# Performance work log

Measured on AMD Instinct MI355X. Metric: run time of the kernel, lower is better.

## Reference

```python
import jax, jax.numpy as jnp
import numpy as np
from jax import lax

# dims
B_SZ, H_SZ, W_SZ = 2, 48, 48
D_MODEL = 192
SSM_RATIO = 2.0
D_PROJ = int(SSM_RATIO * D_MODEL)        # 384
C_INNER = 2 * D_PROJ                     # 768 = K * D_IN
K_GRP = 4
D_IN = C_INNER // K_GRP                  # 192 (= d_inner, channel_divide=2)
N_STATE = 16
R_RANK = 12                              # ceil(192/16)


def setup_inputs() -> dict:
    key = jax.random.key(0)
    ks = jax.random.split(key, 12)
    x = jax.random.normal(ks[0], (B_SZ, H_SZ, W_SZ, 2 * D_MODEL), jnp.float32)
    in_proj_w = jax.random.normal(ks[1], (C_INNER, 2 * D_MODEL), jnp.float32) * 0.02
    conv_w = jax.random.normal(ks[2], (C_INNER, 1, 3, 3), jnp.float32) * 0.1
    conv_b = jnp.zeros((C_INNER,), jnp.float32)
    x_proj_weight = jax.random.normal(ks[3], (K_GRP, R_RANK + 2 * N_STATE, D_IN), jnp.float32) * 0.05
    dt_projs_weight = jax.random.normal(ks[4], (K_GRP, D_IN, R_RANK), jnp.float32) * (R_RANK ** -0.5)
    # faithful dt bias init: softplus^{-1}(dt) with dt ~ logU[1e-3, 1e-1]
    dt = jnp.exp(jax.random.uniform(ks[5], (K_GRP, D_IN)) * (np.log(0.1) - np.log(0.001)) + np.log(0.001))
    dt = jnp.clip(dt, 1e-4, None)
    dt_projs_bias = dt + jnp.log(-jnp.expm1(-dt))
    # A_log init: log(arange(1..N)) per channel, K copies merged
    A_logs = jnp.log(jnp.tile(jnp.arange(1, N_STATE + 1, dtype=jnp.float32)[None, :], (K_GRP * D_IN, 1)))
    Ds = jnp.ones((K_GRP * D_IN,), jnp.float32)
    out_norm_w = jnp.ones((C_INNER,), jnp.float32)
    out_norm_b = jnp.zeros((C_INNER,), jnp.float32)
    out_proj_w = jax.random.normal(ks[6], (2 * D_MODEL, C_INNER), jnp.float32) * 0.02
    return dict(x=x, in_proj_w=in_proj_w, conv_w=conv_w, conv_b=conv_b,
                x_proj_weight=x_proj_weight, dt_projs_weight=dt_projs_weight,
                dt_projs_bias=dt_projs_bias, A_logs=A_logs, Ds=Ds,
                out_norm_w=out_norm_w, out_norm_b=out_norm_b, out_proj_w=out_proj_w)


def _ss2d(x, in_proj_w, conv_w, conv_b, x_proj_weight, dt_projs_weight,
          dt_projs_bias, A_logs, Ds, out_norm_w, out_norm_b, out_proj_w):
    B, H, W, _ = x.shape
    C = in_proj_w.shape[0]
    K = x_proj_weight.shape[0]
    d = C // K
    N = A_logs.shape[1]
    R = dt_projs_weight.shape[2]
    L = H * W

    # in_proj (disable_z: no gating split)
    xz = jnp.einsum('bhwc,oc->bhwo', x, in_proj_w)
    xc = xz.transpose(0, 3, 1, 2)  # [B,C,H,W]
    # depthwise 3x3 conv + SiLU
    xc = lax.conv_general_dilated(xc, conv_w, (1, 1), 'SAME', feature_group_count=C)
    xc = xc + conv_b[None, :, None, None]
    xc = xc * jax.nn.sigmoid(xc)

    # CrossScanS: split channels into K groups, each scanned in its own direction
    ch = xc.reshape(B, K, d, H, W)
    f0 = ch[:, 0].reshape(B, d, L)                                        # row-major fwd
    f1 = ch[:, 1].transpose(0, 1, 3, 2).reshape(B, d, L)                  # col-major fwd
    f2 = jnp.flip(ch[:, 2].reshape(B, d, L), -1)                          # row-major rev
    f3 = jnp.flip(ch[:, 3].transpose(0, 1, 3, 2).reshape(B, d, L), -1)    # col-major rev
    xs = jnp.stack([f0, f1, f2, f3], axis=1)  # [B,K,d,L]

    # input-dependent dt/B/C projections
    x_dbl = jnp.einsum('bkdl,kcd->bkcl', xs, x_proj_weight)
    dts, Bs, Cs = jnp.split(x_dbl, [R, R + N], axis=2)  # [B,K,R,L],[B,K,N,L],[B,K,N,L]
    dts = jnp.einsum('bkrl,kdr->bkdl', dts, dt_projs_weight) + dt_projs_bias[None, :, :, None]

    # force_fp32 selective scan with delta_softplus
    u = xs.astype(jnp.float32)
    dts = jax.nn.softplus(dts.astype(jnp.float32))
    Bs = Bs.astype(jnp.float32)
    Cs = Cs.astype(jnp.float32)
    A = -jnp.exp(A_logs.astype(jnp.float32)).reshape(K, d, N)  # [K,d,N]

    def step(h, inp):
        u_t, dt_t, B_t, C_t = inp  # [B,K,d],[B,K,d],[B,K,N],[B,K,N]
        h = h * jnp.exp(dt_t[..., None] * A) + (dt_t * u_t)[..., None] * B_t[:, :, None, :]
        y_t = jnp.einsum('bkdn,bkn->bkd', h, C_t)
        return h, y_t

    inps = (u.transpose(3, 0, 1, 2), dts.transpose(3, 0, 1, 2),
            Bs.transpose(3, 0, 1, 2), Cs.transpose(3, 0, 1, 2))
    h0 = jnp.zeros((B, K, d, N), jnp.float32)
    _, ys = lax.scan(step, h0, inps)          # ys: [L,B,K,d]
    ys = ys.transpose(1, 2, 3, 0)             # [B,K,d,L]
    ys = ys + Ds.astype(jnp.float32).reshape(K, d)[None, :, :, None] * u

    # CrossMergeS: undo each direction, concat channels back
    y0 = ys[:, 0]
    y1 = ys[:, 1].reshape(B, d, W, H).transpose(0, 1, 3, 2).reshape(B, d, L)
    y2 = jnp.flip(ys[:, 2], -1)
    y3 = jnp.flip(ys[:, 3], -1).reshape(B, d, W, H).transpose(0, 1, 3, 2).reshape(B, d, L)
    y = jnp.concatenate([y0, y1, y2, y3], axis=1).reshape(B, C, H, W).transpose(0, 2, 3, 1)

    # out_norm: LayerNorm over channels
    mu = jnp.mean(y, -1, keepdims=True)
    var = jnp.mean(jnp.square(y - mu), -1, keepdims=True)
    y = (y - mu) * lax.rsqrt(var + 1e-5) * out_norm_w + out_norm_b

    out = jnp.einsum('bhwc,oc->bhwo', y.astype(x.dtype), out_proj_w)
    return out


def reference(x, in_proj_w, conv_w, conv_b, x_proj_weight, dt_projs_weight,
              dt_projs_bias, A_logs, Ds, out_norm_w, out_norm_b, out_proj_w):
    return _ss2d(x, in_proj_w, conv_w, conv_b, x_proj_weight, dt_projs_weight,
                 dt_projs_bias, A_logs, Ds, out_norm_w, out_norm_b, out_proj_w)
```

## Files before the change

kernel.cpp:

```cpp
#include <hip/hip_runtime.h>
#include <hip/hip_bf16.h>

#define B_SZ   2
#define H_SZ   48
#define W_SZ   48
#define L_SZ   2304
#define CIN    768
#define KG     4
#define DI     192
#define NS     16
#define RR     12
#define XD     44
#define MTOK   4608
#define CL     16
#define NC     144

typedef __attribute__((ext_vector_type(8))) short short8;
typedef __attribute__((ext_vector_type(4))) float f32x4;

__device__ inline ushort f2b(float f) {
    uint u = __builtin_bit_cast(uint, f);
    u = (u + 0x7FFF + ((u >> 16) & 1)) >> 16;
    return (ushort)u;
}
__device__ inline float b2f(ushort b) {
    uint u = ((uint)b) << 16;
    return __builtin_bit_cast(float, u);
}
__device__ inline short8 f2b8(float4 a, float4 b) {
    short8 r;
    r[0] = (short)f2b(a.x); r[1] = (short)f2b(a.y);
    r[2] = (short)f2b(a.z); r[3] = (short)f2b(a.w);
    r[4] = (short)f2b(b.x); r[5] = (short)f2b(b.y);
    r[6] = (short)f2b(b.z); r[7] = (short)f2b(b.w);
    return r;
}

__device__ inline void gridbar(uint* bar, uint nb) {
    __syncthreads();
    if (threadIdx.x == 0) {
        uint g = __hip_atomic_load(&bar[1], __ATOMIC_RELAXED, __HIP_MEMORY_SCOPE_AGENT);
        uint a = __hip_atomic_fetch_add(&bar[0], 1u, __ATOMIC_ACQ_REL, __HIP_MEMORY_SCOPE_AGENT);
        if (a == nb - 1u) {
            __hip_atomic_store(&bar[0], 0u, __ATOMIC_RELAXED, __HIP_MEMORY_SCOPE_AGENT);
            __hip_atomic_store(&bar[1], g + 1u, __ATOMIC_RELEASE, __HIP_MEMORY_SCOPE_AGENT);
        } else {
            while (__hip_atomic_load(&bar[1], __ATOMIC_ACQUIRE, __HIP_MEMORY_SCOPE_AGENT) == g) {
                __builtin_amdgcn_s_sleep(8);
            }
        }
    }
    __syncthreads();
}

template<int TM, int TN, bool ABF, bool CBF>
__global__ __launch_bounds__(256) void gemm_tn(
        const void* __restrict__ Av, const float* __restrict__ Bw,
        void* __restrict__ Cv, int M, int N, int K) {
    __shared__ ushort As[TM][72];
    __shared__ ushort Bs[TN][72];
    constexpr int MF   = TM / 64;
    constexpr int NF   = TN / 16;
    constexpr int ANUM = TM / 32;
    constexpr int BNUM = TN / 32;
    const int tid  = threadIdx.x;
    const int lane = tid & 63;
    const int wave = tid >> 6;
    const int wrow = wave * (MF * 16);
    const int bm = blockIdx.y * TM, bn = blockIdx.x * TN;
    const int frow = lane & 15;
    const int fk   = (lane >> 4) * 8;
    const int orow = (lane >> 4) * 4;

    f32x4 acc[MF][NF] = {};

    for (int k0 = 0; k0 < K; k0 += 64) {
        short8 aval[ANUM];
#pragma unroll
        for (int i = 0; i < ANUM; ++i) {
            int idx = tid + i * 256;
            int row = idx >> 3, q = idx & 7;
            if (ABF) {
                aval[i] = *(const short8*)&((const ushort*)Av)[(size_t)(bm + row) * K + k0 + q * 8];
            } else {
                const float* ap = &((const float*)Av)[(size_t)(bm + row) * K + k0 + q * 8];
                aval[i] = f2b8(*(const float4*)ap, *(const float4*)(ap + 4));
            }
        }
        short8 bval[BNUM];
#pragma unroll
        for (int i = 0; i < BNUM; ++i) {
            int idx = tid + i * 256;
            int row = idx >> 3, q = idx & 7;
            const float* bp = &Bw[(size_t)(bn + row) * K + k0 + q * 8];
            bval[i] = f2b8(*(const float4*)bp, *(const float4*)(bp + 4));
        }

        __syncthreads();
#pragma unroll
        for (int i = 0; i < ANUM; ++i) {
            int idx = tid + i * 256;
            *(short8*)&As[idx >> 3][(idx & 7) * 8] = aval[i];
        }
#pragma unroll
        for (int i = 0; i < BNUM; ++i) {
            int idx = tid + i * 256;
            *(short8*)&Bs[idx >> 3][(idx & 7) * 8] = bval[i];
        }
        __syncthreads();

#pragma unroll
        for (int hf = 0; hf < 2; ++hf) {
            short8 af[MF], bf[NF];
#pragma unroll
            for (int mi = 0; mi < MF; ++mi)
                af[mi] = *(const short8*)&As[wrow + mi * 16 + frow][hf * 32 + fk];
#pragma unroll
            for (int ni = 0; ni < NF; ++ni)
                bf[ni] = *(const short8*)&Bs[ni * 16 + frow][hf * 32 + fk];
#pragma unroll
            for (int mi = 0; mi < MF; ++mi)
#pragma unroll
                for (int ni = 0; ni < NF; ++ni)
                    acc[mi][ni] = __builtin_amdgcn_mfma_f32_16x16x32_bf16(
                                      af[mi], bf[ni], acc[mi][ni], 0, 0, 0);
        }
    }

#pragma unroll
    for (int mi = 0; mi < MF; ++mi) {
        int rbase = bm + wrow + mi * 16 + orow;
#pragma unroll
        for (int ni = 0; ni < NF; ++ni) {
            int col = bn + ni * 16 + frow;
#pragma unroll
            for (int r = 0; r < 4; ++r) {
                if (CBF)
                    ((ushort*)Cv)[(size_t)(rbase + r) * N + col] = f2b(acc[mi][ni][r]);
                else
                    ((float*)Cv)[(size_t)(rbase + r) * N + col] = acc[mi][ni][r];
            }
        }
    }
}

__global__ __launch_bounds__(256) void conv_silu_scatter(
        const ushort* __restrict__ xzb, const float* __restrict__ cw,
        const float* __restrict__ cb, ushort* __restrict__ xsb) {
    int g = blockIdx.x * 256 + threadIdx.x;
    int c8 = g % 96;
    int pos = g / 96;
    int w = pos % W_SZ;
    int h = (pos / W_SZ) % H_SZ;
    int b = pos / (W_SZ * H_SZ);
    int c0 = c8 * 8;

    float wt[72];
    const float* cwp = &cw[c0 * 9];
#pragma unroll
    for (int i = 0; i < 18; ++i) {
        float4 v = *(const float4*)(cwp + i * 4);
        wt[i * 4 + 0] = v.x; wt[i * 4 + 1] = v.y;
        wt[i * 4 + 2] = v.z; wt[i * 4 + 3] = v.w;
    }
    float acc[8];
#pragma unroll
    for (int j = 0; j < 8; ++j) acc[j] = cb[c0 + j];

#pragma unroll
    for (int dh = -1; dh <= 1; ++dh) {
        int hh = h + dh;
        if (hh < 0 || hh >= H_SZ) continue;
#pragma unroll
        for (int dw = -1; dw <= 1; ++dw) {
            int ww = w + dw;
            if (ww < 0 || ww >= W_SZ) continue;
            int tap = (dh + 1) * 3 + (dw + 1);
            short8 xv = *(const short8*)&xzb[(size_t)((b * H_SZ + hh) * W_SZ + ww) * CIN + c0];
#pragma unroll
            for (int j = 0; j < 8; ++j)
                acc[j] = fmaf(b2f((ushort)xv[j]), wt[j * 9 + tap], acc[j]);
        }
    }

    float s[8];
#pragma unroll
    for (int j = 0; j < 8; ++j)
        s[j] = acc[j] * __builtin_amdgcn_rcpf(1.f + __expf(-acc[j]));

    int k = c0 / DI, d = c0 % DI;
    int lrow = h * W_SZ + w;
    int lcol = w * H_SZ + h;
    int l;
    if      (k == 0) l = lrow;
    else if (k == 1) l = lcol;
    else if (k == 2) l = L_SZ - 1 - lrow;
    else             l = L_SZ - 1 - lcol;
    float4 lo = {s[0], s[1], s[2], s[3]}, hi = {s[4], s[5], s[6], s[7]};
    *(short8*)&xsb[(size_t)((b * KG + k) * L_SZ + l) * DI + d] = f2b8(lo, hi);
}

__global__ __launch_bounds__(384) void xproj_dt_mfma(
        const ushort* __restrict__ xsb, const float* __restrict__ xpw,
        const float* __restrict__ dtw, const float* __restrict__ dtb,
        float* __restrict__ xdbl, ushort* __restrict__ dts_b) {
    __shared__ ushort Ws[48][200];
    __shared__ ushort Wd[192][40];
    __shared__ ushort dsh[32][40];

    const int tid  = threadIdx.x;
    const int lane = tid & 63;
    const int wave = tid >> 6;
    const int bm = blockIdx.x * 32;
    const int bk = blockIdx.y;
    const int k  = bk & 3;
    const int frow = lane & 15;
    const int fk   = (lane >> 4) * 8;
    const int orow = (lane >> 4) * 4;
    const int rg = wave & 1;
    const int cg = wave >> 1;

#pragma unroll
    for (int i = 0; i < 6; ++i) {
        int idx = tid + i * 384;
        int row = idx / 48, g = idx % 48;
        ushort4 u = {0, 0, 0, 0};
        if (row < XD) {
            float4 v = *(const float4*)&xpw[((size_t)(k * XD) + row) * 192 + g * 4];
            u.x = f2b(v.x); u.y = f2b(v.y); u.z = f2b(v.z); u.w = f2b(v.w);
        }
        *(ushort4*)&Ws[row][g * 4] = u;
    }
#pragma unroll
    for (int i = 0; i < 3; ++i) {
        int idx = tid + i * 384;
        if (idx < 960) {
            float4 z = {0.f, 0.f, 0.f, 0.f};
            *(float4*)&Wd[idx / 5][(idx % 5) * 8] = z;
        } else if (idx < 1120) {
            int j = idx - 960;
            float4 z = {0.f, 0.f, 0.f, 0.f};
            *(float4*)&dsh[j / 5][(j % 5) * 8] = z;
        }
    }
    __syncthreads();

#pragma unroll
    for (int i = 0; i < 6; ++i) {
        int idx = tid + i * 384;
        int row = idx / RR, c = idx % RR;
        Wd[row][c] = f2b(dtw[((size_t)(k * DI) + row) * RR + c]);
    }

    f32x4 acc1 = {};
    const ushort* arow = &xsb[(size_t)(bk * L_SZ + bm + rg * 16 + frow) * DI];
#pragma unroll
    for (int k0 = 0; k0 < 192; k0 += 32) {
        short8 af = *(const short8*)&arow[k0 + fk];
        short8 bv = *(const short8*)&Ws[cg * 16 + frow][k0 + fk];
        acc1 = __builtin_amdgcn_mfma_f32_16x16x32_bf16(af, bv, acc1, 0, 0, 0);
    }

    {
        int col = cg * 16 + frow;
#pragma unroll
        for (int r = 0; r < 4; ++r) {
            float v = acc1[r];
            int row = rg * 16 + orow + r;
            if (col >= RR && col < XD)
                xdbl[(size_t)(bk * L_SZ + bm + row) * XD + col] = v;
            if (cg == 0 && col < RR)
                dsh[row][col] = f2b(v);
        }
    }
    __syncthreads();

#pragma unroll
    for (int t = 0; t < 2; ++t) {
        int d = (wave * 2 + t) * 16 + frow;
        short8 bv = *(const short8*)&Wd[d][fk];
        float bias = dtb[k * DI + d];
#pragma unroll
        for (int rg2 = 0; rg2 < 2; ++rg2) {
            short8 af2 = *(const short8*)&dsh[rg2 * 16 + frow][fk];
            f32x4 a2 = {};
            a2 = __builtin_amdgcn_mfma_f32_16x16x32_bf16(af2, bv, a2, 0, 0, 0);
#pragma unroll
            for (int r = 0; r < 4; ++r) {
                float a = a2[r] + bias;
                float sp = fmaxf(a, 0.f) + __logf(1.f + __expf(-fabsf(a)));
                dts_b[(size_t)(bk * L_SZ + bm + rg2 * 16 + orow + r) * DI + d] = f2b(sp);
            }
        }
    }
}

__global__ __launch_bounds__(192, 4) void scan_fused(
        const ushort* __restrict__ dts_b, const ushort* __restrict__ xsb,
        const float* __restrict__ xdbl, const float* __restrict__ A_logs,
        float* __restrict__ Ebuf, float* __restrict__ Sbuf,
        float* __restrict__ Pbuf, float* __restrict__ Hstart,
        const float* __restrict__ Ds, ushort* __restrict__ ypre_b,
        uint* __restrict__ bar) {
    const int blk = blockIdx.x;
    const int bk = blk / NC, ch = blk % NC;
    const int d = threadIdx.x, k = bk % KG, b = bk / KG;
    const int l0 = ch * CL;

    __shared__ float bsh[CL][NS];
    __shared__ float csh[CL][NS];
    for (int t = threadIdx.x; t < CL * NS; t += 192) {
        int l = t / NS, n = t % NS;
        const float* row = &xdbl[(size_t)(bk * L_SZ + l0 + l) * XD];
        bsh[l][n] = row[RR + n];
        csh[l][n] = row[RR + NS + n];
    }
    __syncthreads();

    {
        float Aa[NS], S[NS];
        const float* ar = &A_logs[(size_t)(k * DI + d) * NS];
        bool fast = true;
#pragma unroll
        for (int n = 0; n < NS; ++n) {
            Aa[n] = -__expf(ar[n]);
            S[n] = 0.f;
            fast = fast && (fabsf(Aa[n] + (float)(n + 1)) < 1e-4f * (n + 1));
        }
        float* sp = &Sbuf[(size_t)((bk * NC + ch) * DI + d) * NS];
        if (fast) {
            float P = 1.f;
#pragma unroll
            for (int l = 0; l < CL; ++l) {
                float dt = b2f(dts_b[(size_t)(bk * L_SZ + l0 + l) * DI + d]);
                float u  = b2f(xsb [(size_t)(bk * L_SZ + l0 + l) * DI + d]);
                float du = dt * u;
                float4 b0 = *(const float4*)&bsh[l][0];
                float4 b1 = *(const float4*)&bsh[l][4];
                float4 b2 = *(const float4*)&bsh[l][8];
                float4 b3 = *(const float4*)&bsh[l][12];
                float Bv[NS] = {b0.x,b0.y,b0.z,b0.w, b1.x,b1.y,b1.z,b1.w,
                                b2.x,b2.y,b2.z,b2.w, b3.x,b3.y,b3.z,b3.w};
                float e1 = __expf(-dt);
                P *= e1;
                float e = e1;
                S[0] = fmaf(S[0], e, du * Bv[0]);
#pragma unroll
                for (int n = 1; n < NS; ++n) {
                    e *= e1;
                    S[n] = fmaf(S[n], e, du * Bv[n]);
                }
            }
            Pbuf[(size_t)(bk * NC + ch) * DI + d] = P;
#pragma unroll
            for (int q = 0; q < 4; ++q) {
                float4 v = {S[q*4], S[q*4+1], S[q*4+2], S[q*4+3]};
                *(float4*)&sp[q * 4] = v;
            }
        } else {
            float E[NS];
#pragma unroll
            for (int n = 0; n < NS; ++n) E[n] = 1.f;
#pragma unroll 8
            for (int l = 0; l < CL; ++l) {
                float dt = b2f(dts_b[(size_t)(bk * L_SZ + l0 + l) * DI + d]);
                float u  = b2f(xsb [(size_t)(bk * L_SZ + l0 + l) * DI + d]);
                float du = dt * u;
                float4 b0 = *(const float4*)&bsh[l][0];
                float4 b1 = *(const float4*)&bsh[l][4];
                float4 b2 = *(const float4*)&bsh[l][8];
                float4 b3 = *(const float4*)&bsh[l][12];
                float Bv[NS] = {b0.x,b0.y,b0.z,b0.w, b1.x,b1.y,b1.z,b1.w,
                                b2.x,b2.y,b2.z,b2.w, b3.x,b3.y,b3.z,b3.w};
#pragma unroll
                for (int n = 0; n < NS; ++n) {
                    float e = __expf(dt * Aa[n]);
                    E[n] *= e;
                    S[n] = fmaf(S[n], e, du * Bv[n]);
                }
            }
            Pbuf[(size_t)(bk * NC + ch) * DI + d] = -1.f;
            float* ep = &Ebuf[(size_t)((bk * NC + ch) * DI + d) * NS];
#pragma unroll
            for (int q = 0; q < 4; ++q) {
                float4 ve = {E[q*4], E[q*4+1], E[q*4+2], E[q*4+3]};
                float4 vs = {S[q*4], S[q*4+1], S[q*4+2], S[q*4+3]};
                *(float4*)&ep[q * 4] = ve;
                *(float4*)&sp[q * 4] = vs;
            }
        }
    }

    gridbar(bar, gridDim.x);

    {
        constexpr int P = 8;
        int t = blk * 192 + threadIdx.x;
        if (t < 8 * DI * 4) {
            int bkB = t / (DI * 4);
            int dn = (t % (DI * 4)) * 4;
            int dB = dn >> 4;
            int n0 = dn & 15;
            const size_t stride = (size_t)DI * NS;
            size_t off = (size_t)(bkB * NC) * stride + dn;
            const float* pb = &Pbuf[(size_t)(bkB * NC) * DI + dB];

            float4 h = {0.f, 0.f, 0.f, 0.f};
            bool fastu = (pb[0] >= 0.f);

            if (fastu) {
                float  pA[P], pB2[P];
                float4 sA[P], sB[P];
                size_t offL = off;
                int    cP   = 0;
#pragma unroll
                for (int j = 0; j < P; ++j) {
                    pA[j] = pb[(size_t)(cP + j) * DI];
                    sA[j] = *(const float4*)&Sbuf[offL + (size_t)j * stride];
                }
                offL += (size_t)P * stride; cP += P;

                for (int c = 0; c < NC; c += 2 * P) {
#pragma unroll
                    for (int j = 0; j < P; ++j) {
                        pB2[j] = pb[(size_t)(cP + j) * DI];
                        sB[j] = *(const float4*)&Sbuf[offL + (size_t)j * stride];
                    }
                    offL += (size_t)P * stride; cP += P;

#pragma unroll
                    for (int j = 0; j < P; ++j) {
                        *(float4*)&Hstart[off + (size_t)j * stride] = h;
                        float Pv = pA[j];
                        float P2 = Pv * Pv, P3 = P2 * Pv;
                        float P4 = P2 * P2, P8 = P4 * P4;
                        float base = Pv * ((n0 & 4) ? P4 : 1.f) * ((n0 & 8) ? P8 : 1.f);
                        h.x = fmaf(base,      h.x, sA[j].x);
                        h.y = fmaf(base * Pv, h.y, sA[j].y);
                        h.z = fmaf(base * P2, h.z, sA[j].z);
                        h.w = fmaf(base * P3, h.w, sA[j].w);
                    }
                    off += (size_t)P * stride;

                    if (c + 2 * P < NC) {
#pragma unroll
                        for (int j = 0; j < P; ++j) {
                            pA[j] = pb[(size_t)(cP + j) * DI];
                            sA[j] = *(const float4*)&Sbuf[offL + (size_t)j * stride];
                        }
                    }
                    offL += (size_t)P * stride; cP += P;

#pragma unroll
                    for (int j = 0; j < P; ++j) {
                        *(float4*)&Hstart[off + (size_t)j * stride] = h;
                        float Pv = pB2[j];
                        float P2 = Pv * Pv, P3 = P2 * Pv;
                        float P4 = P2 * P2, P8 = P4 * P4;
                        float base = Pv * ((n0 & 4) ? P4 : 1.f) * ((n0 & 8) ? P8 : 1.f);
                        h.x = fmaf(base,      h.x, sB[j].x);
                        h.y = fmaf(base * Pv, h.y, sB[j].y);
                        h.z = fmaf(base * P2, h.z, sB[j].z);
                        h.w = fmaf(base * P3, h.w, sB[j].w);
                    }
                    off += (size_t)P * stride;
                }
            } else {
                float4 eA[P], sA[P], eB[P], sB[P];
                size_t offL = off;
#pragma unroll
                for (int j = 0; j < P; ++j) {
                    eA[j] = *(const float4*)&Ebuf[offL + (size_t)j * stride];
                    sA[j] = *(const float4*)&Sbuf[offL + (size_t)j * stride];
                }
                offL += (size_t)P * stride;

                for (int c = 0; c < NC; c += 2 * P) {
#pragma unroll
                    for (int j = 0; j < P; ++j) {
                        eB[j] = *(const float4*)&Ebuf[offL + (size_t)j * stride];
                        sB[j] = *(const float4*)&Sbuf[offL + (size_t)j * stride];
                    }
                    offL += (size_t)P * stride;

#pragma unroll
                    for (int j = 0; j < P; ++j) {
                        *(float4*)&Hstart[off + (size_t)j * stride] = h;
                        h.x = fmaf(eA[j].x, h.x, sA[j].x);
                        h.y = fmaf(eA[j].y, h.y, sA[j].y);
                        h.z = fmaf(eA[j].z, h.z, sA[j].z);
                        h.w = fmaf(eA[j].w, h.w, sA[j].w);
                    }
                    off += (size_t)P * stride;

                    if (c + 2 * P < NC) {
#pragma unroll
                        for (int j = 0; j < P; ++j) {
                            eA[j] = *(const float4*)&Ebuf[offL + (size_t)j * stride];
                            sA[j] = *(const float4*)&Sbuf[offL + (size_t)j * stride];
                        }
                    }
                    offL += (size_t)P * stride;

#pragma unroll
                    for (int j = 0; j < P; ++j) {
                        *(float4*)&Hstart[off + (size_t)j * stride] = h;
                        h.x = fmaf(eB[j].x, h.x, sB[j].x);
                        h.y = fmaf(eB[j].y, h.y, sB[j].y);
                        h.z = fmaf(eB[j].z, h.z, sB[j].z);
                        h.w = fmaf(eB[j].w, h.w, sB[j].w);
                    }
                    off += (size_t)P * stride;
                }
            }
        }
    }

    gridbar(bar, gridDim.x);

    {
        float Aa[NS], h[NS];
        const float* ar = &A_logs[(size_t)(k * DI + d) * NS];
        const float* hp = &Hstart[(size_t)((bk * NC + ch) * DI + d) * NS];
        bool fast = true;
#pragma unroll
        for (int n = 0; n < NS; ++n) {
            Aa[n] = -__expf(ar[n]);
            h[n] = hp[n];
            fast = fast && (fabsf(Aa[n] + (float)(n + 1)) < 1e-4f * (n + 1));
        }
        float Dd = Ds[k * DI + d];

#pragma unroll 8
        for (int l = 0; l < CL; ++l) {
            float dt = b2f(dts_b[(size_t)(bk * L_SZ + l0 + l) * DI + d]);
            float u  = b2f(xsb [(size_t)(bk * L_SZ + l0 + l) * DI + d]);
            float du = dt * u;
            float4 b0 = *(const float4*)&bsh[l][0];
            float4 b1 = *(const float4*)&bsh[l][4];
            float4 b2 = *(const float4*)&bsh[l][8];
            float4 b3 = *(const float4*)&bsh[l][12];
            float Bv[NS] = {b0.x,b0.y,b0.z,b0.w, b1.x,b1.y,b1.z,b1.w,
                            b2.x,b2.y,b2.z,b2.w, b3.x,b3.y,b3.z,b3.w};
            float4 c0 = *(const float4*)&csh[l][0];
            float4 c1 = *(const float4*)&csh[l][4];
            float4 c2 = *(const float4*)&csh[l][8];
            float4 c3 = *(const float4*)&csh[l][12];
            float Cv[NS] = {c0.x,c0.y,c0.z,c0.w, c1.x,c1.y,c1.z,c1.w,
                            c2.x,c2.y,c2.z,c2.w, c3.x,c3.y,c3.z,c3.w};
            float p[NS];
            if (fast) {
                float e1 = __expf(-dt);
                float e = e1;
                h[0] = fmaf(h[0], e, du * Bv[0]);
                p[0] = h[0] * Cv[0];
#pragma unroll
                for (int n = 1; n < NS; ++n) {
                    e *= e1;
                    h[n] = fmaf(h[n], e, du * Bv[n]);
                    p[n] = h[n] * Cv[n];
                }
            } else {
#pragma unroll
                for (int n = 0; n < NS; ++n) {
                    float e = __expf(dt * Aa[n]);
                    h[n] = fmaf(h[n], e, du * Bv[n]);
                    p[n] = h[n] * Cv[n];
                }
            }
#pragma unroll
            for (int s = 8; s >= 1; s >>= 1)
#pragma unroll
                for (int n = 0; n < 8; ++n)
                    if (n < s) p[n] = p[n] + p[n + s];
            float y = fmaf(Dd, u, p[0]);

            int lg = l0 + l;
            int pos;
            if      (k == 0) pos = lg;
            else if (k == 1) pos = (lg % H_SZ) * W_SZ + (lg / H_SZ);
            else if (k == 2) pos = L_SZ - 1 - lg;
            else { int j = L_SZ - 1 - lg; pos = (j % H_SZ) * W_SZ + (j / H_SZ); }
            ypre_b[(size_t)(b * L_SZ + pos) * CIN + k * DI + d] = f2b(y);
        }
    }
}

__global__ __launch_bounds__(192) void scan_passA(
        const ushort* __restrict__ dts_b, const ushort* __restrict__ xsb,
        const float* __restrict__ xdbl, const float* __restrict__ A_logs,
        float* __restrict__ Ebuf, float* __restrict__ Sbuf,
        float* __restrict__ Pbuf) {
    int blk = blockIdx.x;
    int bk = blk / NC, ch = blk % NC;
    int d = threadIdx.x, k = bk % KG;
    int l0 = ch * CL;

    __shared__ float bsh[CL][NS];
    for (int t = threadIdx.x; t < CL * NS; t += 192) {
        int l = t / NS, n = t % NS;
        bsh[l][n] = xdbl[(size_t)(bk * L_SZ + l0 + l) * XD + RR + n];
    }
    __syncthreads();

    float Aa[NS], S[NS];
    const float* ar = &A_logs[(size_t)(k * DI + d) * NS];
    bool fast = true;
#pragma unroll
    for (int n = 0; n < NS; ++n) {
        Aa[n] = -__expf(ar[n]);
        S[n] = 0.f;
        fast = fast && (fabsf(Aa[n] + (float)(n + 1)) < 1e-4f * (n + 1));
    }

    float* sp = &Sbuf[(size_t)((bk * NC + ch) * DI + d) * NS];
    if (fast) {
        float P = 1.f;
#pragma unroll
        for (int l = 0; l < CL; ++l) {
            float dt = b2f(dts_b[(size_t)(bk * L_SZ + l0 + l) * DI + d]);
            float u  = b2f(xsb [(size_t)(bk * L_SZ + l0 + l) * DI + d]);
            float du = dt * u;
            float4 b0 = *(const float4*)&bsh[l][0];
            float4 b1 = *(const float4*)&bsh[l][4];
            float4 b2 = *(const float4*)&bsh[l][8];
            float4 b3 = *(const float4*)&bsh[l][12];
            float Bv[NS] = {b0.x,b0.y,b0.z,b0.w, b1.x,b1.y,b1.z,b1.w,
                            b2.x,b2.y,b2.z,b2.w, b3.x,b3.y,b3.z,b3.w};
            float e1 = __expf(-dt);
            P *= e1;
            float e = e1;
            S[0] = fmaf(S[0], e, du * Bv[0]);
#pragma unroll
            for (int n = 1; n < NS; ++n) {
                e *= e1;
                S[n] = fmaf(S[n], e, du * Bv[n]);
            }
        }
        Pbuf[(size_t)(bk * NC + ch) * DI + d] = P;
#pragma unroll
        for (int q = 0; q < 4; ++q) {
            float4 v = {S[q*4], S[q*4+1], S[q*4+2], S[q*4+3]};
            *(float4*)&sp[q * 4] = v;
        }
    } else {
        float E[NS];
#pragma unroll
        for (int n = 0; n < NS; ++n) E[n] = 1.f;
#pragma unroll 8
        for (int l = 0; l < CL; ++l) {
            float dt = b2f(dts_b[(size_t)(bk * L_SZ + l0 + l) * DI + d]);
            float u  = b2f(xsb [(size_t)(bk * L_SZ + l0 + l) * DI + d]);
            float du = dt * u;
            float4 b0 = *(const float4*)&bsh[l][0];
            float4 b1 = *(const float4*)&bsh[l][4];
            float4 b2 = *(const float4*)&bsh[l][8];
            float4 b3 = *(const float4*)&bsh[l][12];
            float Bv[NS] = {b0.x,b0.y,b0.z,b0.w, b1.x,b1.y,b1.z,b1.w,
                            b2.x,b2.y,b2.z,b2.w, b3.x,b3.y,b3.z,b3.w};
#pragma unroll
            for (int n = 0; n < NS; ++n) {
                float e = __expf(dt * Aa[n]);
                E[n] *= e;
                S[n] = fmaf(S[n], e, du * Bv[n]);
            }
        }
        Pbuf[(size_t)(bk * NC + ch) * DI + d] = -1.f;
        float* ep = &Ebuf[(size_t)((bk * NC + ch) * DI + d) * NS];
#pragma unroll
        for (int q = 0; q < 4; ++q) {
            float4 ve = {E[q*4], E[q*4+1], E[q*4+2], E[q*4+3]};
            float4 vs = {S[q*4], S[q*4+1], S[q*4+2], S[q*4+3]};
            *(float4*)&ep[q * 4] = ve;
            *(float4*)&sp[q * 4] = vs;
        }
    }
}

__global__ __launch_bounds__(64) void scan_passB(
        const float* __restrict__ Ebuf, const float* __restrict__ Sbuf,
        const float* __restrict__ Pbuf, float* __restrict__ Hstart) {
    constexpr int P = 8;
    int t = blockIdx.x * 64 + threadIdx.x;
    int bk = t / (DI * 4);
    int dn = (t % (DI * 4)) * 4;
    int d  = dn >> 4;
    int n0 = dn & 15;
    const size_t stride = (size_t)DI * NS;
    size_t off  = (size_t)(bk * NC) * stride + dn;
    const float* pb = &Pbuf[(size_t)(bk * NC) * DI + d];

    float4 h = {0.f, 0.f, 0.f, 0.f};
    bool fastu = (pb[0] >= 0.f);

    if (fastu) {
        float  pA[P], pB[P];
        float4 sA[P], sB[P];
        size_t offL = off;
        int    cP   = 0;
#pragma unroll
        for (int j = 0; j < P; ++j) {
            pA[j] = pb[(size_t)(cP + j) * DI];
            sA[j] = *(const float4*)&Sbuf[offL + (size_t)j * stride];
        }
        offL += (size_t)P * stride; cP += P;

        for (int c = 0; c < NC; c += 2 * P) {
#pragma unroll
            for (int j = 0; j < P; ++j) {
                pB[j] = pb[(size_t)(cP + j) * DI];
                sB[j] = *(const float4*)&Sbuf[offL + (size_t)j * stride];
            }
            offL += (size_t)P * stride; cP += P;

#pragma unroll
            for (int j = 0; j < P; ++j) {
                *(float4*)&Hstart[off + (size_t)j * stride] = h;
                float Pv = pA[j];
                float P2 = Pv * Pv, P3 = P2 * Pv;
                float P4 = P2 * P2, P8 = P4 * P4;
                float base = Pv * ((n0 & 4) ? P4 : 1.f) * ((n0 & 8) ? P8 : 1.f);
                h.x = fmaf(base,      h.x, sA[j].x);
                h.y = fmaf(base * Pv, h.y, sA[j].y);
                h.z = fmaf(base * P2, h.z, sA[j].z);
                h.w = fmaf(base * P3, h.w, sA[j].w);
            }
            off += (size_t)P * stride;

            if (c + 2 * P < NC) {
#pragma unroll
                for (int j = 0; j < P; ++j) {
                    pA[j] = pb[(size_t)(cP + j) * DI];
                    sA[j] = *(const float4*)&Sbuf[offL + (size_t)j * stride];
                }
            }
            offL += (size_t)P * stride; cP += P;

#pragma unroll
            for (int j = 0; j < P; ++j) {
                *(float4*)&Hstart[off + (size_t)j * stride] = h;
                float Pv = pB[j];
                float P2 = Pv * Pv, P3 = P2 * Pv;
                float P4 = P2 * P2, P8 = P4 * P4;
                float base = Pv * ((n0 & 4) ? P4 : 1.f) * ((n0 & 8) ? P8 : 1.f);
                h.x = fmaf(base,      h.x, sB[j].x);
                h.y = fmaf(base * Pv, h.y, sB[j].y);
                h.z = fmaf(base * P2, h.z, sB[j].z);
                h.w = fmaf(base * P3, h.w, sB[j].w);
            }
            off += (size_t)P * stride;
        }
    } else {
        float4 eA[P], sA[P], eB[P], sB[P];
        size_t offL = off;
#pragma unroll
        for (int j = 0; j < P; ++j) {
            eA[j] = *(const float4*)&Ebuf[offL + (size_t)j * stride];
            sA[j] = *(const float4*)&Sbuf[offL + (size_t)j * stride];
        }
        offL += (size_t)P * stride;

        for (int c = 0; c < NC; c += 2 * P) {
#pragma unroll
            for (int j = 0; j < P; ++j) {
                eB[j] = *(const float4*)&Ebuf[offL + (size_t)j * stride];
                sB[j] = *(const float4*)&Sbuf[offL + (size_t)j * stride];
            }
            offL += (size_t)P * stride;

#pragma unroll
            for (int j = 0; j < P; ++j) {
                *(float4*)&Hstart[off + (size_t)j * stride] = h;
                h.x = fmaf(eA[j].x, h.x, sA[j].x);
                h.y = fmaf(eA[j].y, h.y, sA[j].y);
                h.z = fmaf(eA[j].z, h.z, sA[j].z);
                h.w = fmaf(eA[j].w, h.w, sA[j].w);
            }
            off += (size_t)P * stride;

            if (c + 2 * P < NC) {
#pragma unroll
                for (int j = 0; j < P; ++j) {
                    eA[j] = *(const float4*)&Ebuf[offL + (size_t)j * stride];
                    sA[j] = *(const float4*)&Sbuf[offL + (size_t)j * stride];
                }
            }
            offL += (size_t)P * stride;

#pragma unroll
            for (int j = 0; j < P; ++j) {
                *(float4*)&Hstart[off + (size_t)j * stride] = h;
                h.x = fmaf(eB[j].x, h.x, sB[j].x);
                h.y = fmaf(eB[j].y, h.y, sB[j].y);
                h.z = fmaf(eB[j].z, h.z, sB[j].z);
                h.w = fmaf(eB[j].w, h.w, sB[j].w);
            }
            off += (size_t)P * stride;
        }
    }
}

__global__ __launch_bounds__(192) void scan_passC(
        const ushort* __restrict__ dts_b, const ushort* __restrict__ xsb,
        const float* __restrict__ xdbl, const float* __restrict__ A_logs,
        const float* __restrict__ Hstart, const float* __restrict__ Ds,
        ushort* __restrict__ ypre_b) {
    int blk = blockIdx.x;
    int bk = blk / NC, ch = blk % NC;
    int d = threadIdx.x, k = bk % KG, b = bk / KG;
    int l0 = ch * CL;

    __shared__ float bsh[CL][NS];
    __shared__ float csh[CL][NS];
    for (int t = threadIdx.x; t < CL * NS; t += 192) {
        int l = t / NS, n = t % NS;
        const float* row = &xdbl[(size_t)(bk * L_SZ + l0 + l) * XD];
        bsh[l][n] = row[RR + n];
        csh[l][n] = row[RR + NS + n];
    }
    __syncthreads();

    float Aa[NS], h[NS];
    const float* ar = &A_logs[(size_t)(k * DI + d) * NS];
    const float* hp = &Hstart[(size_t)((bk * NC + ch) * DI + d) * NS];
    bool fast = true;
#pragma unroll
    for (int n = 0; n < NS; ++n) {
        Aa[n] = -__expf(ar[n]);
        h[n] = hp[n];
        fast = fast && (fabsf(Aa[n] + (float)(n + 1)) < 1e-4f * (n + 1));
    }
    float Dd = Ds[k * DI + d];

#pragma unroll 8
    for (int l = 0; l < CL; ++l) {
        float dt = b2f(dts_b[(size_t)(bk * L_SZ + l0 + l) * DI + d]);
        float u  = b2f(xsb [(size_t)(bk * L_SZ + l0 + l) * DI + d]);
        float du = dt * u;
        float4 b0 = *(const float4*)&bsh[l][0];
        float4 b1 = *(const float4*)&bsh[l][4];
        float4 b2 = *(const float4*)&bsh[l][8];
        float4 b3 = *(const float4*)&bsh[l][12];
        float Bv[NS] = {b0.x,b0.y,b0.z,b0.w, b1.x,b1.y,b1.z,b1.w,
                        b2.x,b2.y,b2.z,b2.w, b3.x,b3.y,b3.z,b3.w};
        float4 c0 = *(const float4*)&csh[l][0];
        float4 c1 = *(const float4*)&csh[l][4];
        float4 c2 = *(const float4*)&csh[l][8];
        float4 c3 = *(const float4*)&csh[l][12];
        float Cv[NS] = {c0.x,c0.y,c0.z,c0.w, c1.x,c1.y,c1.z,c1.w,
                        c2.x,c2.y,c2.z,c2.w, c3.x,c3.y,c3.z,c3.w};
        float p[NS];
        if (fast) {
            float e1 = __expf(-dt);
            float e = e1;
            h[0] = fmaf(h[0], e, du * Bv[0]);
            p[0] = h[0] * Cv[0];
#pragma unroll
            for (int n = 1; n < NS; ++n) {
                e *= e1;
                h[n] = fmaf(h[n], e, du * Bv[n]);
                p[n] = h[n] * Cv[n];
            }
        } else {
#pragma unroll
            for (int n = 0; n < NS; ++n) {
                float e = __expf(dt * Aa[n]);
                h[n] = fmaf(h[n], e, du * Bv[n]);
                p[n] = h[n] * Cv[n];
            }
        }
#pragma unroll
        for (int s = 8; s >= 1; s >>= 1)
#pragma unroll
            for (int n = 0; n < 8; ++n)
                if (n < s) p[n] = p[n] + p[n + s];
        float y = fmaf(Dd, u, p[0]);

        int lg = l0 + l;
        int pos;
        if      (k == 0) pos = lg;
        else if (k == 1) pos = (lg % H_SZ) * W_SZ + (lg / H_SZ);
        else if (k == 2) pos = L_SZ - 1 - lg;
        else { int j = L_SZ - 1 - lg; pos = (j % H_SZ) * W_SZ + (j / H_SZ); }
        ypre_b[(size_t)(b * L_SZ + pos) * CIN + k * DI + d] = f2b(y);
    }
}

__global__ __launch_bounds__(256) void layernorm_bf16(
        const ushort* __restrict__ y, ushort* __restrict__ yb,
        const float* __restrict__ w, const float* __restrict__ bg) {
    int wave = threadIdx.x >> 6, lane = threadIdx.x & 63;
    int tok = blockIdx.x * 4 + wave;
    const ushort* row = &y[(size_t)tok * CIN];
    ushort* rowo = &yb[(size_t)tok * CIN];
    float v[12];
    float s = 0.f;
#pragma unroll
    for (int i = 0; i < 12; ++i) { v[i] = b2f(row[lane + i * 64]); s += v[i]; }
#pragma unroll
    for (int off = 32; off >= 1; off >>= 1) s += __shfl_xor(s, off, 64);
    float mu = s * (1.f / CIN);
    float s2 = 0.f;
#pragma unroll
    for (int i = 0; i < 12; ++i) { float t = v[i] - mu; s2 += t * t; }
#pragma unroll
    for (int off = 32; off >= 1; off >>= 1) s2 += __shfl_xor(s2, off, 64);
    float rstd = rsqrtf(s2 * (1.f / CIN) + 1e-5f);
#pragma unroll
    for (int i = 0; i < 12; ++i)
        rowo[lane + i * 64] =
            f2b((v[i] - mu) * rstd * w[lane + i * 64] + bg[lane + i * 64]);
}

extern "C" void kernel_launch(void* const* d_in, const int* in_sizes, int n_in,
                              void* d_out, int out_size, void* d_ws, size_t ws_size,
                              hipStream_t stream) {
    const float* x    = (const float*)d_in[0];
    const float* inw  = (const float*)d_in[1];
    const float* cw   = (const float*)d_in[2];
    const float* cb   = (const float*)d_in[3];
    const float* xpw  = (const float*)d_in[4];
    const float* dtw  = (const float*)d_in[5];
    const float* dtb  = (const float*)d_in[6];
    const float* alog = (const float*)d_in[7];
    const float* Dsp  = (const float*)d_in[8];
    const float* lnw  = (const float*)d_in[9];
    const float* lnb  = (const float*)d_in[10];
    const float* outw = (const float*)d_in[11];
    float* out = (float*)d_out;

    float* ws = (float*)d_ws;
    const size_t SZ_BIG = (size_t)MTOK * CIN;
    const size_t SCAN_SL = (size_t)8 * NC * DI * NS;
    float* xz    = ws;
    float* xsbf  = xz  + SZ_BIG;
    float* dts   = xsbf + SZ_BIG / 2;
    float* xdbl  = dts + SZ_BIG;
    float* Ebuf  = xdbl + (size_t)8 * L_SZ * XD;
    float* Sbuf  = Ebuf + SCAN_SL;
    float* Hst   = Sbuf + SCAN_SL;
    float* Pbuf  = Hst + SCAN_SL;
    uint*  bar   = (uint*)(Pbuf + (size_t)8 * NC * DI);
    ushort* xzb    = (ushort*)xz;
    ushort* xsb    = (ushort*)xsbf;
    ushort* dtsb   = (ushort*)dts;
    ushort* ypre_b = (ushort*)xz;
    ushort* ynrm_b = (ushort*)dts;

    gemm_tn<64, 64, false, true><<<dim3(CIN / 64, MTOK / 64), 256, 0, stream>>>(
        x, inw, xzb, MTOK, CIN, 384);
    conv_silu_scatter<<<(B_SZ * H_SZ * W_SZ * 96) / 256, 256, 0, stream>>>(xzb, cw, cb, xsb);
    xproj_dt_mfma<<<dim3(L_SZ / 32, 8), 384, 0, stream>>>(xsb, xpw, dtw, dtb, xdbl, dtsb);

    int maxb = 0;
    hipError_t oe = hipOccupancyMaxActiveBlocksPerMultiprocessor(
        &maxb, scan_fused, 192, 0);
    if (oe == hipSuccess && maxb * 256 >= 8 * NC) {
        hipMemsetAsync(bar, 0, 2 * sizeof(uint), stream);
        scan_fused<<<8 * NC, 192, 0, stream>>>(
            dtsb, xsb, xdbl, alog, Ebuf, Sbuf, Pbuf, Hst, Dsp, ypre_b, bar);
    } else {
        scan_passA<<<8 * NC, 192, 0, stream>>>(dtsb, xsb, xdbl, alog, Ebuf, Sbuf, Pbuf);
        scan_passB<<<(8 * DI * 4) / 64, 64, 0, stream>>>(Ebuf, Sbuf, Pbuf, Hst);
        scan_passC<<<8 * NC, 192, 0, stream>>>(dtsb, xsb, xdbl, alog, Hst, Dsp, ypre_b);
    }
    layernorm_bf16<<<MTOK / 4, 256, 0, stream>>>(ypre_b, ynrm_b, lnw, lnb);
    gemm_tn<64, 32, true, false><<<dim3(384 / 32, MTOK / 64), 256, 0, stream>>>(
        ynrm_b, outw, out, MTOK, 384, CIN);
}
```

Before: 178.9 us.

## Fuse layernorm into scan via grid barrier and pre-convert GEMM inputs to bf16

Adds a kernel that converts x, in_proj and out_proj weights to bf16 in one pass, so both GEMMs load bf16 operands directly instead of converting fp32 on every tile load. LayerNorm is folded into the persistent scan kernel after an extra grid barrier, where each block normalizes 4 tokens, removing one kernel launch and a separate pass over the scan output. The cost is an extra conversion launch, extra workspace, and one more grid-wide sync inside the scan.

```diff
diff --git a/kernel.cpp b/kernel.cpp
--- a/kernel.cpp
+++ b/kernel.cpp
@@ -14,6 +14,8 @@
 #define MTOK   4608
 #define CL     16
 #define NC     144
+#define NXF    (MTOK * 384)
+#define NWF    (CIN * 384)
 
 typedef __attribute__((ext_vector_type(8))) short short8;
 typedef __attribute__((ext_vector_type(4))) float f32x4;
@@ -34,6 +36,20 @@
     r[4] = (short)f2b(b.x); r[5] = (short)f2b(b.y);
     r[6] = (short)f2b(b.z); r[7] = (short)f2b(b.w);
     return r;
+}
+
+__global__ __launch_bounds__(256) void to_bf16_3(
+        const float* __restrict__ x, const float* __restrict__ inw,
+        const float* __restrict__ outw, ushort* __restrict__ xb,
+        ushort* __restrict__ inwb, ushort* __restrict__ outwb) {
+    int i4 = (blockIdx.x * 256 + threadIdx.x) * 4;
+    const float* src; ushort* dst; int off;
+    if (i4 < NXF)             { src = x;    dst = xb;    off = i4; }
+    else if (i4 < NXF + NWF)  { src = inw;  dst = inwb;  off = i4 - NXF; }
+    else                      { src = outw; dst = outwb; off = i4 - NXF - NWF; }
+    float4 v = *(const float4*)&src[off];
+    ushort4 u = {f2b(v.x), f2b(v.y), f2b(v.z), f2b(v.w)};
+    *(ushort4*)&dst[off] = u;
 }
 
 __device__ inline void gridbar(uint* bar, uint nb) {
@@ -53,9 +69,9 @@
     __syncthreads();
 }
 
-template<int TM, int TN, bool ABF, bool CBF>
+template<int TM, int TN, bool ABF, bool BBF, bool CBF>
 __global__ __launch_bounds__(256) void gemm_tn(
-        const void* __restrict__ Av, const float* __restrict__ Bw,
+        const void* __restrict__ Av, const void* __restrict__ Bw,
         void* __restrict__ Cv, int M, int N, int K) {
     __shared__ ushort As[TM][72];
     __shared__ ushort Bs[TN][72];
@@ -92,8 +108,12 @@
         for (int i = 0; i < BNUM; ++i) {
             int idx = tid + i * 256;
             int row = idx >> 3, q = idx & 7;
-            const float* bp = &Bw[(size_t)(bn + row) * K + k0 + q * 8];
-            bval[i] = f2b8(*(const float4*)bp, *(const float4*)(bp + 4));
+            if (BBF) {
+                bval[i] = *(const short8*)&((const ushort*)Bw)[(size_t)(bn + row) * K + k0 + q * 8];
+            } else {
+                const float* bp = &((const float*)Bw)[(size_t)(bn + row) * K + k0 + q * 8];
+                bval[i] = f2b8(*(const float4*)bp, *(const float4*)(bp + 4));
+            }
         }
 
         __syncthreads();
@@ -301,7 +321,8 @@
         float* __restrict__ Ebuf, float* __restrict__ Sbuf,
         float* __restrict__ Pbuf, float* __restrict__ Hstart,
         const float* __restrict__ Ds, ushort* __restrict__ ypre_b,
-        uint* __restrict__ bar) {
+        const float* __restrict__ lnw, const float* __restrict__ lnb,
+        ushort* __restrict__ ynrm_b, uint* __restrict__ bar) {
     const int blk = blockIdx.x;
     const int bk = blk / NC, ch = blk % NC;
     const int d = threadIdx.x, k = bk % KG, b = bk / KG;
@@ -309,6 +330,7 @@
 
     __shared__ float bsh[CL][NS];
     __shared__ float csh[CL][NS];
+    __shared__ float red[2][3];
     for (int t = threadIdx.x; t < CL * NS; t += 192) {
         int l = t / NS, n = t % NS;
         const float* row = &xdbl[(size_t)(bk * L_SZ + l0 + l) * XD];
@@ -584,6 +606,40 @@
             ypre_b[(size_t)(b * L_SZ + pos) * CIN + k * DI + d] = f2b(y);
         }
     }
+
+    gridbar(bar, gridDim.x);
+
+    {
+        int lane = threadIdx.x & 63, wv = threadIdx.x >> 6;
+        int i4 = threadIdx.x * 4;
+        float4 w4 = *(const float4*)&lnw[i4];
+        float4 g4 = *(const float4*)&lnb[i4];
+        for (int j = 0; j < 4; ++j) {
+            int tok = blk * 4 + j;
+            ushort4 rv = *(const ushort4*)&ypre_b[(size_t)tok * CIN + i4];
+            float v0 = b2f(rv.x), v1 = b2f(rv.y), v2 = b2f(rv.z), v3 = b2f(rv.w);
+            float s1 = v0 + v1 + v2 + v3;
+            float s2 = v0*v0 + v1*v1 + v2*v2 + v3*v3;
+#pragma unroll
+            for (int off = 32; off >= 1; off >>= 1) {
+                s1 += __shfl_xor(s1, off, 64);
+                s2 += __shfl_xor(s2, off, 64);
+            }
+            if (lane == 0) { red[0][wv] = s1; red[1][wv] = s2; }
+            __syncthreads();
+            float ts1 = red[0][0] + red[0][1] + red[0][2];
+            float ts2 = red[1][0] + red[1][1] + red[1][2];
+            float mu = ts1 * (1.f / CIN);
+            float rstd = rsqrtf(ts2 * (1.f / CIN) - mu * mu + 1e-5f);
+            ushort4 o;
+            o.x = f2b((v0 - mu) * rstd * w4.x + g4.x);
+            o.y = f2b((v1 - mu) * rstd * w4.y + g4.y);
+            o.z = f2b((v2 - mu) * rstd * w4.z + g4.z);
+            o.w = f2b((v3 - mu) * rstd * w4.w + g4.w);
+            *(ushort4*)&ynrm_b[(size_t)tok * CIN + i4] = o;
+            __syncthreads();
+        }
+    }
 }
 
 __global__ __launch_bounds__(192) void scan_passA(
@@ -940,15 +996,19 @@
     float* Sbuf  = Ebuf + SCAN_SL;
     float* Hst   = Sbuf + SCAN_SL;
     float* Pbuf  = Hst + SCAN_SL;
-    uint*  bar   = (uint*)(Pbuf + (size_t)8 * NC * DI);
+    ushort* xb   = (ushort*)(Pbuf + (size_t)8 * NC * DI);
+    ushort* inwb = xb + NXF;
+    ushort* outwb= inwb + NWF;
+    uint*  bar   = (uint*)(outwb + NWF);
     ushort* xzb    = (ushort*)xz;
     ushort* xsb    = (ushort*)xsbf;
     ushort* dtsb   = (ushort*)dts;
     ushort* ypre_b = (ushort*)xz;
     ushort* ynrm_b = (ushort*)dts;
 
-    gemm_tn<64, 64, false, true><<<dim3(CIN / 64, MTOK / 64), 256, 0, stream>>>(
-        x, inw, xzb, MTOK, CIN, 384);
+    to_bf16_3<<<(NXF + 2 * NWF) / 1024, 256, 0, stream>>>(x, inw, outw, xb, inwb, outwb);
+    gemm_tn<64, 64, true, true, true><<<dim3(CIN / 64, MTOK / 64), 256, 0, stream>>>(
+        xb, inwb, xzb, MTOK, CIN, 384);
     conv_silu_scatter<<<(B_SZ * H_SZ * W_SZ * 96) / 256, 256, 0, stream>>>(xzb, cw, cb, xsb);
     xproj_dt_mfma<<<dim3(L_SZ / 32, 8), 384, 0, stream>>>(xsb, xpw, dtw, dtb, xdbl, dtsb);
 
@@ -958,13 +1018,14 @@
     if (oe == hipSuccess && maxb * 256 >= 8 * NC) {
         hipMemsetAsync(bar, 0, 2 * sizeof(uint), stream);
         scan_fused<<<8 * NC, 192, 0, stream>>>(
-            dtsb, xsb, xdbl, alog, Ebuf, Sbuf, Pbuf, Hst, Dsp, ypre_b, bar);
+            dtsb, xsb, xdbl, alog, Ebuf, Sbuf, Pbuf, Hst, Dsp, ypre_b,
+            lnw, lnb, ynrm_b, bar);
     } else {
         scan_passA<<<8 * NC, 192, 0, stream>>>(dtsb, xsb, xdbl, alog, Ebuf, Sbuf, Pbuf);
         scan_passB<<<(8 * DI * 4) / 64, 64, 0, stream>>>(Ebuf, Sbuf, Pbuf, Hst);
         scan_passC<<<8 * NC, 192, 0, stream>>>(dtsb, xsb, xdbl, alog, Hst, Dsp, ypre_b);
-    }
-    layernorm_bf16<<<MTOK / 4, 256, 0, stream>>>(ypre_b, ynrm_b, lnw, lnb);
-    gemm_tn<64, 32, true, false><<<dim3(384 / 32, MTOK / 64), 256, 0, stream>>>(
-        ynrm_b, outw, out, MTOK, 384, CIN);
-}
+        layernorm_bf16<<<MTOK / 4, 256, 0, stream>>>(ypre_b, ynrm_b, lnw, lnb);
+    }
+    gemm_tn<64, 32, true, true, false><<<dim3(384 / 32, MTOK / 64), 256, 0, stream>>>(
+        ynrm_b, outwb, out, MTOK, 384, CIN);
+}
```

Result: no change. 177.1 us (-1.0%).
